# Kernel tuning notes

Measured on AMD Instinct MI355X. Metric: run time of the kernel, lower is better.

Reference implementation:

```python
import jax, jax.numpy as jnp
import numpy as np

D_MODEL = 1024
D_STATE = 32
EXPAND = 2
D_INNER = D_MODEL * EXPAND          # 2048
DT_RANK = D_MODEL // 16             # 64
LN_EPS = 1e-5


def setup_inputs() -> dict:
    key = jax.random.key(0)
    ks = jax.random.split(key, 9)
    s = 0.02
    x = jax.random.normal(ks[0], (2, 2048, D_MODEL), dtype=jnp.float32)
    W_in = jax.random.normal(ks[1], (2 * D_INNER, D_MODEL), dtype=jnp.float32) * s
    W_x = jax.random.normal(ks[2], (DT_RANK + 2 * D_STATE, D_INNER), dtype=jnp.float32) * s
    W_dt = jax.random.normal(ks[3], (D_INNER, DT_RANK), dtype=jnp.float32) * s
    b_dt = jax.random.normal(ks[4], (D_INNER,), dtype=jnp.float32) * s
    A_real0 = jax.random.normal(ks[5], (D_INNER, D_STATE), dtype=jnp.float32) * 0.5
    A_log_real = jnp.log(jnp.clip(-A_real0, 1e-4, None))
    A_imag = jax.random.normal(ks[6], (D_INNER, D_STATE), dtype=jnp.float32) * 0.1
    D_param = jnp.ones((D_INNER,), dtype=jnp.float32)
    W_out = jax.random.normal(ks[7], (D_MODEL, D_INNER), dtype=jnp.float32) * s
    ln_g = jnp.ones((D_MODEL,), dtype=jnp.float32)
    ln_b = jnp.zeros((D_MODEL,), dtype=jnp.float32)
    return {"x": x, "W_in": W_in, "W_x": W_x, "W_dt": W_dt, "b_dt": b_dt,
            "A_log_real": A_log_real, "A_imag": A_imag, "D_param": D_param,
            "W_out": W_out, "ln_g": ln_g, "ln_b": ln_b}


def _forward(x, W_in, W_x, W_dt, b_dt, A_log_real, A_imag, D_param, W_out, ln_g, ln_b):
    B, T, _ = x.shape
    residual = x
    # LayerNorm
    mu = jnp.mean(x, axis=-1, keepdims=True)
    var = jnp.mean((x - mu) ** 2, axis=-1, keepdims=True)
    xn = (x - mu) * jax.lax.rsqrt(var + LN_EPS) * ln_g + ln_b
    # in_proj -> (x_ssm, z)
    xz = jnp.einsum('btd,ed->bte', xn, W_in)            # (B,T,2*d_inner)
    x_ssm, z = jnp.split(xz, 2, axis=-1)
    # x_proj -> dt_low, B, C
    x_dbl = jnp.einsum('bte,re->btr', x_ssm, W_x)        # (B,T,dt_rank+2*d_state)
    dt_low = x_dbl[..., :DT_RANK]
    B_param = x_dbl[..., DT_RANK:DT_RANK + D_STATE]      # (B,T,N)
    C_param = x_dbl[..., DT_RANK + D_STATE:]             # (B,T,N)
    dt = jax.nn.softplus(jnp.einsum('btr,er->bte', dt_low, W_dt) + b_dt)  # (B,T,d_inner)
    # A = -exp(A_log_real) + i * A_imag, complex state split into (hr, hi)
    Ar = -jnp.exp(A_log_real)                             # (d_inner,N)
    Ai = A_imag

    def step(carry, inp):
        hr, hi = carry                                    # (B,d_inner,N)
        dt_t, B_t, C_t, x_t = inp                         # (B,d_inner),(B,N),(B,N),(B,d_inner)
        dtE = dt_t[:, :, None]                            # (B,d_inner,1)
        scale = jnp.exp(Ar[None] * dtE)
        ang = Ai[None] * dtE
        dAr = scale * jnp.cos(ang)
        dAi = scale * jnp.sin(ang)
        dBx = (dt_t * x_t)[:, :, None] * B_t[:, None, :]  # real input injection
        hr2 = dAr * hr - dAi * hi + dBx
        hi2 = dAr * hi + dAi * hr
        y = jnp.sum(hr2 * C_t[:, None, :], axis=-1)       # real part of (h * C).sum
        return (hr2, hi2), y

    h0 = jnp.zeros((B, D_INNER, D_STATE), dtype=x.dtype)
    xs = (jnp.transpose(dt, (1, 0, 2)), jnp.transpose(B_param, (1, 0, 2)),
          jnp.transpose(C_param, (1, 0, 2)), jnp.transpose(x_ssm, (1, 0, 2)))
    _, ys = jax.lax.scan(step, (h0, h0), xs)              # (T,B,d_inner)
    y = jnp.transpose(ys, (1, 0, 2)) + D_param * x_ssm
    y = y * jax.nn.silu(z)
    out = jnp.einsum('bte,de->btd', y, W_out)
    return residual + out  # dropout is identity at eval


def reference(x, W_in, W_x, W_dt, b_dt, A_log_real, A_imag, D_param, W_out, ln_g, ln_b):
    return _forward(x, W_in, W_x, W_dt, b_dt, A_log_real, A_imag, D_param, W_out, ln_g, ln_b)
```

## Files before the change

### kernel.cpp

```cpp
#include <hip/hip_runtime.h>
#include <math.h>

#define D_MODEL 1024
#define D_STATE 32
#define D_INNER 2048
#define DT_RANK 64
#define BT 4096
#define XZLD 4224
#define LN_EPS 1e-5f

typedef __attribute__((ext_vector_type(8))) short short8;
typedef __attribute__((ext_vector_type(4))) float f32x4;
typedef const __attribute__((address_space(1))) void* gp_t;
typedef __attribute__((address_space(3))) void* lp_t;

__device__ __forceinline__ ushort bf16r(float f) {
    unsigned u = __float_as_uint(f);
    u += 0x7fff + ((u >> 16) & 1);
    return (ushort)(u >> 16);
}

__device__ __forceinline__ float dpp_red32(float x) {
    int t;
    t = __builtin_amdgcn_update_dpp(0, __float_as_int(x), 0x111, 0xf, 0xf, true);
    x += __int_as_float(t);
    t = __builtin_amdgcn_update_dpp(0, __float_as_int(x), 0x112, 0xf, 0xf, true);
    x += __int_as_float(t);
    t = __builtin_amdgcn_update_dpp(0, __float_as_int(x), 0x114, 0xf, 0xf, true);
    x += __int_as_float(t);
    t = __builtin_amdgcn_update_dpp(0, __float_as_int(x), 0x118, 0xf, 0xf, true);
    x += __int_as_float(t);
    t = __builtin_amdgcn_update_dpp(0, __float_as_int(x), 0x142, 0xa, 0xf, true);
    x += __int_as_float(t);
    return x;
}

__global__ __launch_bounds__(256) void cvt_bf16(const float* __restrict__ in,
                                                ushort* __restrict__ out, int n4) {
    int i = blockIdx.x * 256 + threadIdx.x;
    if (i >= n4) return;
    float4 v = ((const float4*)in)[i];
    ushort4 o;
    o.x = bf16r(v.x); o.y = bf16r(v.y); o.z = bf16r(v.z); o.w = bf16r(v.w);
    ((ushort4*)out)[i] = o;
}

__global__ __launch_bounds__(256) void cvt_dtlow(const float* __restrict__ xz,
                                                 ushort* __restrict__ out) {
    int i = blockIdx.x * 256 + threadIdx.x;
    int row = i >> 4, c = (i & 15) << 2;
    float4 v = *(const float4*)&xz[(size_t)row * XZLD + 4096 + c];
    ushort4 o;
    o.x = bf16r(v.x); o.y = bf16r(v.y); o.z = bf16r(v.z); o.w = bf16r(v.w);
    ((ushort4*)out)[i] = o;
}

__global__ __launch_bounds__(256) void transpose_cvt(const float* __restrict__ in,
                                                     ushort* __restrict__ out) {
    __shared__ float tile[32][33];
    int bx = blockIdx.x * 32;
    int by = blockIdx.y * 32;
    int tx = threadIdx.x & 31, ty = threadIdx.x >> 5;
    #pragma unroll
    for (int i = 0; i < 32; i += 8)
        tile[ty + i][tx] = in[(size_t)(bx + ty + i) * 1024 + by + tx];
    __syncthreads();
    #pragma unroll
    for (int i = 0; i < 32; i += 8)
        out[(size_t)(by + ty + i) * 2048 + bx + tx] = bf16r(tile[tx][ty + i]);
}

__global__ __launch_bounds__(256) void ln_kernel(const float* __restrict__ x,
                                                 const float* __restrict__ g,
                                                 const float* __restrict__ b,
                                                 ushort* __restrict__ xn) {
    int row = blockIdx.x;
    const float4* xr = (const float4*)(x + (size_t)row * D_MODEL);
    float4 v = xr[threadIdx.x];
    float s  = v.x + v.y + v.z + v.w;
    float ss = v.x*v.x + v.y*v.y + v.z*v.z + v.w*v.w;
    #pragma unroll
    for (int off = 32; off > 0; off >>= 1) {
        s  += __shfl_down(s,  off, 64);
        ss += __shfl_down(ss, off, 64);
    }
    __shared__ float rs[4], rss[4];
    int wave = threadIdx.x >> 6;
    if ((threadIdx.x & 63) == 0) { rs[wave] = s; rss[wave] = ss; }
    __syncthreads();
    s  = rs[0] + rs[1] + rs[2] + rs[3];
    ss = rss[0] + rss[1] + rss[2] + rss[3];
    float mu  = s * (1.f / D_MODEL);
    float var = ss * (1.f / D_MODEL) - mu * mu;
    float inv = rsqrtf(var + LN_EPS);
    float4 gv = ((const float4*)g)[threadIdx.x];
    float4 bv = ((const float4*)b)[threadIdx.x];
    ushort4 o;
    o.x = bf16r((v.x - mu) * inv * gv.x + bv.x);
    o.y = bf16r((v.y - mu) * inv * gv.y + bv.y);
    o.z = bf16r((v.z - mu) * inv * gv.z + bv.z);
    o.w = bf16r((v.w - mu) * inv * gv.w + bv.w);
    ((ushort4*)(xn + (size_t)row * D_MODEL))[threadIdx.x] = o;
}

template<int RESID, int ACT>
__global__ __launch_bounds__(256) void gemm_bt_bf16(
    const ushort* __restrict__ A, const ushort* __restrict__ B,
    float* __restrict__ C, int ldc, int K,
    const float* __restrict__ resid, const float* __restrict__ bias)
{
    __shared__ __align__(16) ushort As[128 * 32];
    __shared__ __align__(16) ushort Bs[128 * 32];
    int tid = threadIdx.x;
    int bm = blockIdx.x * 128, bn = blockIdx.y * 128;
    int wave = tid >> 6, lane = tid & 63;
    int wm = (wave & 1) * 64, wn = (wave >> 1) * 64;
    int quad = lane >> 4, m16 = lane & 15;
    int grow = tid >> 2;
    int gcol = (tid & 3) * 8;
    const size_t a0 = (size_t)(bm + grow) * K + gcol;
    const size_t b0 = (size_t)(bn + grow) * K + gcol;
    char* asw = (char*)As + wave * 1024;
    char* bsw = (char*)Bs + wave * 1024;

    f32x4 acc[4][4] = {};
    for (int k0 = 0; k0 < K; k0 += 32) {
        __builtin_amdgcn_global_load_lds((gp_t)(A + a0 + k0),                 (lp_t)asw,          16, 0, 0);
        __builtin_amdgcn_global_load_lds((gp_t)(A + a0 + (size_t)64*K + k0),  (lp_t)(asw + 4096), 16, 0, 0);
        __builtin_amdgcn_global_load_lds((gp_t)(B + b0 + k0),                 (lp_t)bsw,          16, 0, 0);
        __builtin_amdgcn_global_load_lds((gp_t)(B + b0 + (size_t)64*K + k0),  (lp_t)(bsw + 4096), 16, 0, 0);
        __syncthreads();
        short8 af[4], bf[4];
        #pragma unroll
        for (int i = 0; i < 4; ++i)
            af[i] = *(const short8*)&As[(wm + i * 16 + m16) * 32 + quad * 8];
        #pragma unroll
        for (int j = 0; j < 4; ++j)
            bf[j] = *(const short8*)&Bs[(wn + j * 16 + m16) * 32 + quad * 8];
        #pragma unroll
        for (int i = 0; i < 4; ++i)
            #pragma unroll
            for (int j = 0; j < 4; ++j)
                acc[i][j] = __builtin_amdgcn_mfma_f32_16x16x32_bf16(
                    af[i], bf[j], acc[i][j], 0, 0, 0);
        __syncthreads();
    }
    #pragma unroll
    for (int i = 0; i < 4; ++i) {
        #pragma unroll
        for (int r = 0; r < 4; ++r) {
            int row = bm + wm + i * 16 + quad * 4 + r;
            #pragma unroll
            for (int j = 0; j < 4; ++j) {
                int col = bn + wn + j * 16 + m16;
                float v = acc[i][j][r];
                if (ACT == 1) {
                    v += bias[col];
                    v = (v > 20.f) ? v : __logf(1.f + __expf(v));
                }
                if (RESID) v += resid[(size_t)row * ldc + col];
                C[(size_t)row * ldc + col] = v;
            }
        }
    }
}

__global__ __launch_bounds__(256) void scan_kernel(
    const float* __restrict__ xz,
    const float* __restrict__ dtm,
    const float* __restrict__ A_log_real,
    const float* __restrict__ A_imag,
    const float* __restrict__ D_param,
    ushort* __restrict__ y)
{
    const int tid  = threadIdx.x;
    const int s    = tid & 31;
    const int el   = tid >> 5;
    const int b    = blockIdx.x >> 8;
    const int e0   = (blockIdx.x & 255) << 3;
    const int e    = e0 + el;
    const int sk   = tid & 7;
    const int stt  = tid >> 3;
    const int brow = tid >> 4;
    const int bcp  = tid & 15;

    __shared__ __align__(16) float dxp[2][8][17][4];
    __shared__ __align__(16) float xzs[2][8][34][2];
    __shared__ __align__(16) float bcs[2][32][68];

    const float Ar2  = -__expf(A_log_real[e * D_STATE + s]) * 1.44269504f;
    const float Ai2p = A_imag[e * D_STATE + s] * 0.15915494f;
    const float Dps  = D_param[e0 + sk];
    float hr = 0.f, hi = 0.f;
    const float* xzb = xz + (size_t)b * 2048 * XZLD;
    const float* bcb = xzb + 4096 + DT_RANK;
    const float* dtb = dtm + (size_t)b * 2048 * 2048;
    ushort*      yb  = y   + (size_t)b * 2048 * 2048;

    float r_d, r_x, r_z;
    float2 rb0, rc0, rb1, rc1;
    {
        r_d = dtb[(size_t)stt * 2048 + e0 + sk];
        r_x = xzb[(size_t)stt * XZLD + e0 + sk];
        r_z = xzb[(size_t)stt * XZLD + 2048 + e0 + sk];
        rb0 = *(const float2*)&bcb[(size_t)brow * XZLD + 2 * bcp];
        rc0 = *(const float2*)&bcb[(size_t)brow * XZLD + 32 + 2 * bcp];
        rb1 = *(const float2*)&bcb[(size_t)(brow + 16) * XZLD + 2 * bcp];
        rc1 = *(const float2*)&bcb[(size_t)(brow + 16) * XZLD + 32 + 2 * bcp];
        float dtx = r_d * r_x;
        float g   = r_z / (1.f + __expf(-r_z));
        float Dx  = Dps * r_x;
        *(float2*)&dxp[0][sk][stt >> 1][(stt & 1) * 2] = make_float2(r_d, dtx);
        *(float2*)&xzs[0][sk][stt]                     = make_float2(Dx, g);
        *(float4*)&bcs[0][brow][4 * bcp]      = make_float4(rb0.x, rc0.x, rb0.y, rc0.y);
        *(float4*)&bcs[0][brow + 16][4 * bcp] = make_float4(rb1.x, rc1.x, rb1.y, rc1.y);
    }
    for (int c = 0; c < 64; ++c) {
        const int buf = c & 1;
        __syncthreads();
        if (c < 63) {
            const int tn = (c + 1) * 32;
            r_d = dtb[(size_t)(tn + stt) * 2048 + e0 + sk];
            r_x = xzb[(size_t)(tn + stt) * XZLD + e0 + sk];
            r_z = xzb[(size_t)(tn + stt) * XZLD + 2048 + e0 + sk];
            rb0 = *(const float2*)&bcb[(size_t)(tn + brow) * XZLD + 2 * bcp];
            rc0 = *(const float2*)&bcb[(size_t)(tn + brow) * XZLD + 32 + 2 * bcp];
            rb1 = *(const float2*)&bcb[(size_t)(tn + brow + 16) * XZLD + 2 * bcp];
            rc1 = *(const float2*)&bcb[(size_t)(tn + brow + 16) * XZLD + 32 + 2 * bcp];
        }
        #pragma unroll 4
        for (int tp = 0; tp < 16; ++tp) {
            float4 dd  = *(const float4*)&dxp[buf][el][tp][0];
            float2 bc0 = *(const float2*)&bcs[buf][2 * tp][2 * s];
            float2 bc1 = *(const float2*)&bcs[buf][2 * tp + 1][2 * s];
            float sc = __builtin_amdgcn_exp2f(Ar2 * dd.x);
            float u  = Ai2p * dd.x;
            float sa = __builtin_amdgcn_sinf(u), ca = __builtin_amdgcn_cosf(u);
            float dAr = sc * ca, dAi = sc * sa;
            float hrn = fmaf(dAr, hr, fmaf(-dAi, hi, dd.y * bc0.x));
            hi = fmaf(dAr, hi, dAi * hr); hr = hrn;
            float p0 = hr * bc0.y;
            sc = __builtin_amdgcn_exp2f(Ar2 * dd.z);
            u  = Ai2p * dd.z;
            sa = __builtin_amdgcn_sinf(u); ca = __builtin_amdgcn_cosf(u);
            dAr = sc * ca; dAi = sc * sa;
            hrn = fmaf(dAr, hr, fmaf(-dAi, hi, dd.w * bc1.x));
            hi = fmaf(dAr, hi, dAi * hr); hr = hrn;
            float p1 = hr * bc1.y;
            p0 = dpp_red32(p0);
            p1 = dpp_red32(p1);
            if (s == 31) {
                float4 xg = *(const float4*)&xzs[buf][el][2 * tp];
                yb[(size_t)(c * 32 + 2 * tp) * 2048 + e]     = bf16r((p0 + xg.x) * xg.y);
                yb[(size_t)(c * 32 + 2 * tp + 1) * 2048 + e] = bf16r((p1 + xg.z) * xg.w);
            }
        }
        if (c < 63) {
            const int nb = buf ^ 1;
            float dtx = r_d * r_x;
            float g   = r_z / (1.f + __expf(-r_z));
            float Dx  = Dps * r_x;
            *(float2*)&dxp[nb][sk][stt >> 1][(stt & 1) * 2] = make_float2(r_d, dtx);
            *(float2*)&xzs[nb][sk][stt]                     = make_float2(Dx, g);
            *(float4*)&bcs[nb][brow][4 * bcp]      = make_float4(rb0.x, rc0.x, rb0.y, rc0.y);
            *(float4*)&bcs[nb][brow + 16][4 * bcp] = make_float4(rb1.x, rc1.x, rb1.y, rc1.y);
        }
    }
}

extern "C" void kernel_launch(void* const* d_in, const int* in_sizes, int n_in,
                              void* d_out, int out_size, void* d_ws, size_t ws_size,
                              hipStream_t stream) {
    const float* x          = (const float*)d_in[0];
    const float* W_in       = (const float*)d_in[1];
    const float* W_x        = (const float*)d_in[2];
    const float* W_dt       = (const float*)d_in[3];
    const float* b_dt       = (const float*)d_in[4];
    const float* A_log_real = (const float*)d_in[5];
    const float* A_imag     = (const float*)d_in[6];
    const float* D_param    = (const float*)d_in[7];
    const float* W_out      = (const float*)d_in[8];
    const float* ln_g       = (const float*)d_in[9];
    const float* ln_b       = (const float*)d_in[10];
    float* out = (float*)d_out;

    char* ws = (char*)d_ws;
    float*  xz       = (float*) (ws);
    float*  dt       = (float*) (ws + ((size_t) 66 << 20));
    ushort* xn_bf    = (ushort*)(ws + ((size_t) 98 << 20));
    ushort* Waug     = (ushort*)(ws + ((size_t)106 << 20));
    ushort* y_bf     = (ushort*)(ws + ((size_t)115 << 20));
    ushort* Wout_bf  = (ushort*)(ws + ((size_t)131 << 20));
    ushort* Wdt_bf   = (ushort*)(ws + ((size_t)135 << 20));
    ushort* dtlow_bf = (ushort*)(ws + ((size_t)136 << 20));
    float*  Wcomb   = (float*) (ws);
    ushort* Wx_bf   = (ushort*)(ws + ((size_t)  1 << 20));
    ushort* WinT_bf = (ushort*)(ws + ((size_t)  2 << 20));

    cvt_bf16<<<4096, 256, 0, stream>>>(W_in,  Waug,    4096*1024/4);
    cvt_bf16<<<2048, 256, 0, stream>>>(W_out, Wout_bf, 1024*2048/4);
    cvt_bf16<<< 256, 256, 0, stream>>>(W_x,   Wx_bf,    128*2048/4);
    cvt_bf16<<< 128, 256, 0, stream>>>(W_dt,  Wdt_bf,   2048*64/4);
    transpose_cvt<<<dim3(64, 32), 256, 0, stream>>>(W_in, WinT_bf);
    gemm_bt_bf16<0,0><<<dim3(1, 8), 256, 0, stream>>>(
        Wx_bf, WinT_bf, Wcomb, 1024, 2048, nullptr, nullptr);
    cvt_bf16<<<128, 256, 0, stream>>>(Wcomb, Waug + (size_t)4096*1024, 128*1024/4);
    ln_kernel<<<BT, 256, 0, stream>>>(x, ln_g, ln_b, xn_bf);
    gemm_bt_bf16<0,0><<<dim3(BT/128, XZLD/128), 256, 0, stream>>>(
        xn_bf, Waug, xz, XZLD, D_MODEL, nullptr, nullptr);
    cvt_dtlow<<<256, 256, 0, stream>>>(xz, dtlow_bf);
    gemm_bt_bf16<0,1><<<dim3(BT/128, D_INNER/128), 256, 0, stream>>>(
        dtlow_bf, Wdt_bf, dt, D_INNER, DT_RANK, nullptr, b_dt);
    scan_kernel<<<512, 256, 0, stream>>>(xz, dt, A_log_real, A_imag, D_param, y_bf);
    gemm_bt_bf16<1,0><<<dim3(BT/128, D_MODEL/128), 256, 0, stream>>>(
        y_bf, Wout_bf, out, D_MODEL, D_INNER, x, nullptr);
}
```

Measured before the change: 552.2 us.

## Restructure scan reduction via shared partials and fuse weight conversion launches

The scan kernel now reduces over 16 lanes with DPP, then stores per-half partial sums in shared memory. It writes each chunk's y outputs at the end with all 32 lanes instead of one lane per step, and the B/C shared layout is changed so one float4 load serves both timesteps. The four weight conversion kernels are merged into one launch, and the combined-weight GEMM writes bf16 directly, removing an extra conversion kernel. This aims to cut serialized single-lane stores and cross-row DPP cost in the scan, at the price of extra shared memory traffic and a full inner-loop unroll.

```diff
diff --git a/kernel.cpp b/kernel.cpp
--- a/kernel.cpp
+++ b/kernel.cpp
@@ -20,7 +20,7 @@
     return (ushort)(u >> 16);
 }
 
-__device__ __forceinline__ float dpp_red32(float x) {
+__device__ __forceinline__ float dpp_red16(float x) {
     int t;
     t = __builtin_amdgcn_update_dpp(0, __float_as_int(x), 0x111, 0xf, 0xf, true);
     x += __int_as_float(t);
@@ -30,19 +30,24 @@
     x += __int_as_float(t);
     t = __builtin_amdgcn_update_dpp(0, __float_as_int(x), 0x118, 0xf, 0xf, true);
     x += __int_as_float(t);
-    t = __builtin_amdgcn_update_dpp(0, __float_as_int(x), 0x142, 0xa, 0xf, true);
-    x += __int_as_float(t);
     return x;
 }
 
-__global__ __launch_bounds__(256) void cvt_bf16(const float* __restrict__ in,
-                                                ushort* __restrict__ out, int n4) {
-    int i = blockIdx.x * 256 + threadIdx.x;
-    if (i >= n4) return;
-    float4 v = ((const float4*)in)[i];
+__global__ __launch_bounds__(256) void prep_weights(
+    const float* __restrict__ W_in, const float* __restrict__ W_out,
+    const float* __restrict__ W_dt, const float* __restrict__ W_x,
+    ushort* __restrict__ Waug, ushort* __restrict__ Wout_bf,
+    ushort* __restrict__ Wdt_bf, ushort* __restrict__ Wx_bf) {
+    int bid = blockIdx.x;
+    const float* src; ushort* dst; int i;
+    if (bid < 4096)      { src = W_in;  dst = Waug;    i = bid * 256 + threadIdx.x; }
+    else if (bid < 6144) { src = W_out; dst = Wout_bf; i = (bid - 4096) * 256 + threadIdx.x; }
+    else if (bid < 6400) { src = W_x;   dst = Wx_bf;   i = (bid - 6144) * 256 + threadIdx.x; }
+    else                 { src = W_dt;  dst = Wdt_bf;  i = (bid - 6400) * 256 + threadIdx.x; }
+    float4 v = ((const float4*)src)[i];
     ushort4 o;
     o.x = bf16r(v.x); o.y = bf16r(v.y); o.z = bf16r(v.z); o.w = bf16r(v.w);
-    ((ushort4*)out)[i] = o;
+    ((ushort4*)dst)[i] = o;
 }
 
 __global__ __launch_bounds__(256) void cvt_dtlow(const float* __restrict__ xz,
@@ -103,10 +108,10 @@
     ((ushort4*)(xn + (size_t)row * D_MODEL))[threadIdx.x] = o;
 }
 
-template<int RESID, int ACT>
+template<int RESID, int ACT, int OBF>
 __global__ __launch_bounds__(256) void gemm_bt_bf16(
     const ushort* __restrict__ A, const ushort* __restrict__ B,
-    float* __restrict__ C, int ldc, int K,
+    void* __restrict__ Cv, int ldc, int K,
     const float* __restrict__ resid, const float* __restrict__ bias)
 {
     __shared__ __align__(16) ushort As[128 * 32];
@@ -159,7 +164,8 @@
                     v = (v > 20.f) ? v : __logf(1.f + __expf(v));
                 }
                 if (RESID) v += resid[(size_t)row * ldc + col];
-                C[(size_t)row * ldc + col] = v;
+                if (OBF) ((ushort*)Cv)[(size_t)row * ldc + col] = bf16r(v);
+                else     ((float*) Cv)[(size_t)row * ldc + col] = v;
             }
         }
     }
@@ -174,19 +180,20 @@
     ushort* __restrict__ y)
 {
     const int tid  = threadIdx.x;
+    const int lane = tid & 63;
     const int s    = tid & 31;
-    const int el   = tid >> 5;
+    const int elb  = tid >> 5;
     const int b    = blockIdx.x >> 8;
     const int e0   = (blockIdx.x & 255) << 3;
-    const int e    = e0 + el;
-    const int sk   = tid & 7;
-    const int stt  = tid >> 3;
-    const int brow = tid >> 4;
-    const int bcp  = tid & 15;
+    const int e    = e0 + elb;
+    const int stt  = tid >> 3, sk  = tid & 7;
+    const int btp  = tid >> 4, bsp = tid & 15;
+    const int q    = (lane >> 4) & 1;
 
     __shared__ __align__(16) float dxp[2][8][17][4];
     __shared__ __align__(16) float xzs[2][8][34][2];
-    __shared__ __align__(16) float bcs[2][32][68];
+    __shared__ __align__(16) float bcs[2][16][33][4];
+    __shared__ __align__(16) float pp[8][2][32];
 
     const float Ar2  = -__expf(A_log_real[e * D_STATE + s]) * 1.44269504f;
     const float Ai2p = A_imag[e * D_STATE + s] * 0.15915494f;
@@ -198,74 +205,65 @@
     ushort*      yb  = y   + (size_t)b * 2048 * 2048;
 
     float r_d, r_x, r_z;
-    float2 rb0, rc0, rb1, rc1;
-    {
-        r_d = dtb[(size_t)stt * 2048 + e0 + sk];
-        r_x = xzb[(size_t)stt * XZLD + e0 + sk];
-        r_z = xzb[(size_t)stt * XZLD + 2048 + e0 + sk];
-        rb0 = *(const float2*)&bcb[(size_t)brow * XZLD + 2 * bcp];
-        rc0 = *(const float2*)&bcb[(size_t)brow * XZLD + 32 + 2 * bcp];
-        rb1 = *(const float2*)&bcb[(size_t)(brow + 16) * XZLD + 2 * bcp];
-        rc1 = *(const float2*)&bcb[(size_t)(brow + 16) * XZLD + 32 + 2 * bcp];
-        float dtx = r_d * r_x;
-        float g   = r_z / (1.f + __expf(-r_z));
-        float Dx  = Dps * r_x;
-        *(float2*)&dxp[0][sk][stt >> 1][(stt & 1) * 2] = make_float2(r_d, dtx);
-        *(float2*)&xzs[0][sk][stt]                     = make_float2(Dx, g);
-        *(float4*)&bcs[0][brow][4 * bcp]      = make_float4(rb0.x, rc0.x, rb0.y, rc0.y);
-        *(float4*)&bcs[0][brow + 16][4 * bcp] = make_float4(rb1.x, rc1.x, rb1.y, rc1.y);
-    }
+    float2 rB0, rC0, rB1, rC1;
+
+#define LOADC(T0) do {                                                        \
+    r_d = dtb[(size_t)((T0) + stt) * 2048 + e0 + sk];                         \
+    r_x = xzb[(size_t)((T0) + stt) * XZLD + e0 + sk];                         \
+    r_z = xzb[(size_t)((T0) + stt) * XZLD + 2048 + e0 + sk];                  \
+    rB0 = *(const float2*)&bcb[(size_t)((T0) + 2*btp) * XZLD + 2*bsp];        \
+    rC0 = *(const float2*)&bcb[(size_t)((T0) + 2*btp) * XZLD + 32 + 2*bsp];   \
+    rB1 = *(const float2*)&bcb[(size_t)((T0) + 2*btp+1) * XZLD + 2*bsp];      \
+    rC1 = *(const float2*)&bcb[(size_t)((T0) + 2*btp+1) * XZLD + 32 + 2*bsp]; \
+  } while (0)
+
+#define STAGE(NB) do {                                                        \
+    float dtx = r_d * r_x;                                                    \
+    float gg  = r_z / (1.f + __expf(-r_z));                                   \
+    float Dx  = Dps * r_x;                                                    \
+    *(float2*)&dxp[NB][sk][stt >> 1][(stt & 1) * 2] = make_float2(r_d, dtx);  \
+    *(float2*)&xzs[NB][sk][stt] = make_float2(Dx, gg);                        \
+    *(float4*)&bcs[NB][btp][2*bsp][0]   = make_float4(rB0.x, rC0.x, rB1.x, rC1.x); \
+    *(float4*)&bcs[NB][btp][2*bsp+1][0] = make_float4(rB0.y, rC0.y, rB1.y, rC1.y); \
+  } while (0)
+
+    LOADC(0);
+    STAGE(0);
     for (int c = 0; c < 64; ++c) {
         const int buf = c & 1;
         __syncthreads();
-        if (c < 63) {
-            const int tn = (c + 1) * 32;
-            r_d = dtb[(size_t)(tn + stt) * 2048 + e0 + sk];
-            r_x = xzb[(size_t)(tn + stt) * XZLD + e0 + sk];
-            r_z = xzb[(size_t)(tn + stt) * XZLD + 2048 + e0 + sk];
-            rb0 = *(const float2*)&bcb[(size_t)(tn + brow) * XZLD + 2 * bcp];
-            rc0 = *(const float2*)&bcb[(size_t)(tn + brow) * XZLD + 32 + 2 * bcp];
-            rb1 = *(const float2*)&bcb[(size_t)(tn + brow + 16) * XZLD + 2 * bcp];
-            rc1 = *(const float2*)&bcb[(size_t)(tn + brow + 16) * XZLD + 32 + 2 * bcp];
-        }
-        #pragma unroll 4
+        if (c < 63) LOADC((c + 1) * 32);
+        #pragma unroll
         for (int tp = 0; tp < 16; ++tp) {
-            float4 dd  = *(const float4*)&dxp[buf][el][tp][0];
-            float2 bc0 = *(const float2*)&bcs[buf][2 * tp][2 * s];
-            float2 bc1 = *(const float2*)&bcs[buf][2 * tp + 1][2 * s];
+            float4 dd = *(const float4*)&dxp[buf][elb][tp][0];
+            float4 bc = *(const float4*)&bcs[buf][tp][s][0];
             float sc = __builtin_amdgcn_exp2f(Ar2 * dd.x);
             float u  = Ai2p * dd.x;
             float sa = __builtin_amdgcn_sinf(u), ca = __builtin_amdgcn_cosf(u);
             float dAr = sc * ca, dAi = sc * sa;
-            float hrn = fmaf(dAr, hr, fmaf(-dAi, hi, dd.y * bc0.x));
+            float hrn = fmaf(dAr, hr, fmaf(-dAi, hi, dd.y * bc.x));
             hi = fmaf(dAr, hi, dAi * hr); hr = hrn;
-            float p0 = hr * bc0.y;
+            float p0 = hr * bc.y;
             sc = __builtin_amdgcn_exp2f(Ar2 * dd.z);
             u  = Ai2p * dd.z;
             sa = __builtin_amdgcn_sinf(u); ca = __builtin_amdgcn_cosf(u);
             dAr = sc * ca; dAi = sc * sa;
-            hrn = fmaf(dAr, hr, fmaf(-dAi, hi, dd.w * bc1.x));
+            hrn = fmaf(dAr, hr, fmaf(-dAi, hi, dd.w * bc.z));
             hi = fmaf(dAr, hi, dAi * hr); hr = hrn;
-            float p1 = hr * bc1.y;
-            p0 = dpp_red32(p0);
-            p1 = dpp_red32(p1);
-            if (s == 31) {
-                float4 xg = *(const float4*)&xzs[buf][el][2 * tp];
-                yb[(size_t)(c * 32 + 2 * tp) * 2048 + e]     = bf16r((p0 + xg.x) * xg.y);
-                yb[(size_t)(c * 32 + 2 * tp + 1) * 2048 + e] = bf16r((p1 + xg.z) * xg.w);
-            }
+            float p1 = hr * bc.w;
+            p0 = dpp_red16(p0);
+            p1 = dpp_red16(p1);
+            if ((lane & 15) == 15)
+                *(float2*)&pp[elb][q][2 * tp] = make_float2(p0, p1);
         }
-        if (c < 63) {
-            const int nb = buf ^ 1;
-            float dtx = r_d * r_x;
-            float g   = r_z / (1.f + __expf(-r_z));
-            float Dx  = Dps * r_x;
-            *(float2*)&dxp[nb][sk][stt >> 1][(stt & 1) * 2] = make_float2(r_d, dtx);
-            *(float2*)&xzs[nb][sk][stt]                     = make_float2(Dx, g);
-            *(float4*)&bcs[nb][brow][4 * bcp]      = make_float4(rb0.x, rc0.x, rb0.y, rc0.y);
-            *(float4*)&bcs[nb][brow + 16][4 * bcp] = make_float4(rb1.x, rc1.x, rb1.y, rc1.y);
-        }
+        float pA = pp[elb][0][s];
+        float pB = pp[elb][1][s];
+        float2 xg = *(const float2*)&xzs[buf][elb][s];
+        yb[(size_t)(c * 32 + s) * 2048 + e] = bf16r((pA + pB + xg.x) * xg.y);
+        if (c < 63) STAGE(buf ^ 1);
     }
+#undef LOADC
+#undef STAGE
 }
 
 extern "C" void kernel_launch(void* const* d_in, const int* in_sizes, int n_in,
@@ -293,25 +291,21 @@
     ushort* Wout_bf  = (ushort*)(ws + ((size_t)131 << 20));
     ushort* Wdt_bf   = (ushort*)(ws + ((size_t)135 << 20));
     ushort* dtlow_bf = (ushort*)(ws + ((size_t)136 << 20));
-    float*  Wcomb   = (float*) (ws);
     ushort* Wx_bf   = (ushort*)(ws + ((size_t)  1 << 20));
     ushort* WinT_bf = (ushort*)(ws + ((size_t)  2 << 20));
 
-    cvt_bf16<<<4096, 256, 0, stream>>>(W_in,  Waug,    4096*1024/4);
-    cvt_bf16<<<2048, 256, 0, stream>>>(W_out, Wout_bf, 1024*2048/4);
-    cvt_bf16<<< 256, 256, 0, stream>>>(W_x,   Wx_bf,    128*2048/4);
-    cvt_bf16<<< 128, 256, 0, stream>>>(W_dt,  Wdt_bf,   2048*64/4);
+    prep_weights<<<6528, 256, 0, stream>>>(W_in, W_out, W_dt, W_x,
+                                           Waug, Wout_bf, Wdt_bf, Wx_bf);
     transpose_cvt<<<dim3(64, 32), 256, 0, stream>>>(W_in, WinT_bf);
-    gemm_bt_bf16<0,0><<<dim3(1, 8), 256, 0, stream>>>(
-        Wx_bf, WinT_bf, Wcomb, 1024, 2048, nullptr, nullptr);
-    cvt_bf16<<<128, 256, 0, stream>>>(Wcomb, Waug + (size_t)4096*1024, 128*1024/4);
+    gemm_bt_bf16<0,0,1><<<dim3(1, 8), 256, 0, stream>>>(
+        Wx_bf, WinT_bf, Waug + (size_t)4096 * 1024, 1024, 2048, nullptr, nullptr);
     ln_kernel<<<BT, 256, 0, stream>>>(x, ln_g, ln_b, xn_bf);
-    gemm_bt_bf16<0,0><<<dim3(BT/128, XZLD/128), 256, 0, stream>>>(
+    gemm_bt_bf16<0,0,0><<<dim3(BT/128, XZLD/128), 256, 0, stream>>>(
         xn_bf, Waug, xz, XZLD, D_MODEL, nullptr, nullptr);
     cvt_dtlow<<<256, 256, 0, stream>>>(xz, dtlow_bf);
-    gemm_bt_bf16<0,1><<<dim3(BT/128, D_INNER/128), 256, 0, stream>>>(
+    gemm_bt_bf16<0,1,0><<<dim3(BT/128, D_INNER/128), 256, 0, stream>>>(
         dtlow_bf, Wdt_bf, dt, D_INNER, DT_RANK, nullptr, b_dt);
     scan_kernel<<<512, 256, 0, stream>>>(xz, dt, A_log_real, A_imag, D_param, y_bf);
-    gemm_bt_bf16<1,0><<<dim3(BT/128, D_MODEL/128), 256, 0, stream>>>(
+    gemm_bt_bf16<1,0,0><<<dim3(BT/128, D_MODEL/128), 256, 0, stream>>>(
         y_bf, Wout_bf, out, D_MODEL, D_INNER, x, nullptr);
 }
```

Result: faster. 501.7 us (-9.1%).
